# Kernel optimization log

Measured on AMD Instinct MI355X. Metric: run time of the kernel, lower is better.

The kernel has to match this reference:

```python
import jax, jax.numpy as jnp
import numpy as np

N = 50000
E = 800000
IN_DIM = 128
HEADS = 8
OUT_DIM = 32
NEG_SLOPE = 0.2


def setup_inputs() -> dict:
    key = jax.random.key(0)
    k1, k2, k3, k4, k5 = jax.random.split(key, 5)
    x = jax.random.normal(k1, (N, IN_DIM), dtype=jnp.float32)
    edge_index = jax.random.randint(k2, (2, E), 0, N, dtype=jnp.int64)
    batch = jnp.zeros((N,), dtype=jnp.int64)
    # GATConv params: glorot-style scale
    W = jax.random.normal(k3, (IN_DIM, HEADS * OUT_DIM), dtype=jnp.float32) * (1.0 / np.sqrt(IN_DIM))
    att_src = jax.random.normal(k4, (HEADS, OUT_DIM), dtype=jnp.float32) * (1.0 / np.sqrt(OUT_DIM))
    att_dst = jax.random.normal(k5, (HEADS, OUT_DIM), dtype=jnp.float32) * (1.0 / np.sqrt(OUT_DIM))
    bias = jnp.zeros((OUT_DIM,), dtype=jnp.float32)
    return {"x": x, "edge_index": edge_index, "batch": batch,
            "W": W, "att_src": att_src, "att_dst": att_dst, "bias": bias}


def reference(x, edge_index, batch, W, att_src, att_dst, bias):
    n = x.shape[0]
    h = (x @ W).reshape(n, HEADS, OUT_DIM)            # [N, H, C]
    a_src = jnp.einsum('nhc,hc->nh', h, att_src)       # [N, H]
    a_dst = jnp.einsum('nhc,hc->nh', h, att_dst)       # [N, H]
    # add self-loops (PyG default add_self_loops=True)
    loops = jnp.arange(n, dtype=edge_index.dtype)
    src = jnp.concatenate([edge_index[0], loops])
    dst = jnp.concatenate([edge_index[1], loops])
    e = jax.nn.leaky_relu(a_src[src] + a_dst[dst], NEG_SLOPE)  # [E+N, H]
    # scatter-softmax over incoming edges of each dst node
    m = jax.ops.segment_max(e, dst, num_segments=n)    # [N, H]
    m = jax.lax.stop_gradient(m)
    ex = jnp.exp(e - m[dst])
    denom = jax.ops.segment_sum(ex, dst, num_segments=n)
    alpha = ex / denom[dst]                            # [E+N, H]
    msg = h[src] * alpha[..., None]                    # [E+N, H, C]
    out = jax.ops.segment_sum(msg, dst, num_segments=n)  # [N, H, C]
    out = out.mean(axis=1) + bias                      # concat=False -> head mean
    return out
```

## Files before the change

### kernel.cpp

```cpp
#include <hip/hip_runtime.h>
#include <hip/hip_bf16.h>

#define IN_DIM 128
#define HC 256
#define HEADS 8
#define OUT_DIM 32
#define NEG_SLOPE 0.2f
#define ELL_CAP 64

typedef unsigned short ushort_t;
typedef unsigned int uint_t;
typedef __attribute__((ext_vector_type(8))) short bf16x8;
typedef __attribute__((ext_vector_type(8))) unsigned short ushort8_t;
typedef __attribute__((ext_vector_type(4))) float floatx4;

__device__ inline ushort_t f2bf(float f) {
    uint_t u = __float_as_uint(f);
    u = (u + 0x7FFF + ((u >> 16) & 1)) >> 16;
    return (ushort_t)u;
}
__device__ inline float bf2f(ushort_t u) {
    return __uint_as_float(((uint_t)u) << 16);
}
__device__ inline uint_t pkbf(float a, float b) {
    __hip_bfloat162 t = __float22bfloat162_rn(make_float2(a, b));
    union { __hip_bfloat162 h; uint_t u; } c;
    c.h = t;
    return c.u;
}

__global__ __launch_bounds__(256) void prep_w_zero(const float* __restrict__ W,
                                                   ushort_t* __restrict__ Wf,
                                                   int* __restrict__ deg, int N) {
    const int t = blockIdx.x * 256 + threadIdx.x;
    for (int i = t; i < N; i += 4096) deg[i] = 0;

    int lane = t & 63;
    int ks = (t >> 6) & 3;
    int nt = t >> 8;
    int n = nt * 16 + (lane & 15);
    int k0 = ks * 32 + (lane >> 4) * 8;
    float v[8];
#pragma unroll
    for (int j = 0; j < 8; j++) v[j] = W[(size_t)(k0 + j) * HC + n];
    uint4 pk;
    pk.x = pkbf(v[0], v[1]);
    pk.y = pkbf(v[2], v[3]);
    pk.z = pkbf(v[4], v[5]);
    pk.w = pkbf(v[6], v[7]);
    *(uint4*)&Wf[(size_t)t * 8] = pk;
}

__global__ __launch_bounds__(256) void build_gemm(const float* __restrict__ x,
                                                  const ushort_t* __restrict__ Wf,
                                                  const float* __restrict__ att_s,
                                                  const float* __restrict__ att_d,
                                                  ushort_t* __restrict__ h2,
                                                  float* __restrict__ a_src,
                                                  float* __restrict__ a_dst,
                                                  const int* __restrict__ esrc,
                                                  const int* __restrict__ edst,
                                                  int* __restrict__ deg,
                                                  ushort_t* __restrict__ ell,
                                                  int N, int E, int nbuild) {
    __shared__ ushort_t xs[128 * 136];
    const int tid = threadIdx.x;

    if ((int)blockIdx.x < nbuild) {
        int i = blockIdx.x * 256 + tid;
        int base = i * 4;
        if (base + 3 < E) {
            int4 d = *(const int4*)&edst[base];
            int4 s = *(const int4*)&esrc[base];
            int r0 = atomicAdd(&deg[d.x], 1);
            int r1 = atomicAdd(&deg[d.y], 1);
            int r2 = atomicAdd(&deg[d.z], 1);
            int r3 = atomicAdd(&deg[d.w], 1);
            if (r0 < ELL_CAP) ell[d.x * ELL_CAP + r0] = (ushort_t)s.x;
            if (r1 < ELL_CAP) ell[d.y * ELL_CAP + r1] = (ushort_t)s.y;
            if (r2 < ELL_CAP) ell[d.z * ELL_CAP + r2] = (ushort_t)s.z;
            if (r3 < ELL_CAP) ell[d.w * ELL_CAP + r3] = (ushort_t)s.w;
        } else if (base < E) {
            for (int j = base; j < E; j++) {
                int r = atomicAdd(&deg[edst[j]], 1);
                if (r < ELL_CAP) ell[edst[j] * ELL_CAP + r] = (ushort_t)esrc[j];
            }
        }
        return;
    }

    const int row0 = ((int)blockIdx.x - nbuild) * 128;
#pragma unroll
    for (int i = 0; i < 16; i++) {
        int slot = tid + i * 256;
        int r = slot >> 5, kq = slot & 31;
        int gr = row0 + r;
        float4 v = (gr < N) ? *(const float4*)&x[(size_t)gr * IN_DIM + kq * 4]
                            : make_float4(0.f, 0.f, 0.f, 0.f);
        uint2 pk;
        pk.x = pkbf(v.x, v.y);
        pk.y = pkbf(v.z, v.w);
        *(uint2*)&xs[r * 136 + kq * 4] = pk;
    }
    __syncthreads();

    const int lane = tid & 63;
    const int w = tid >> 6;
    const int wrow = (w & 1) * 64;
    const int wcol = (w >> 1) * 64;
    const int m15 = lane & 15, quad = lane >> 4;

#pragma unroll
    for (int ch = 0; ch < 2; ch++) {
        const int colblk = wcol + ch * 128;
        floatx4 acc[4][4] = {};
#pragma unroll
        for (int ks = 0; ks < 4; ks++) {
            bf16x8 xb[4], wa[4];
#pragma unroll
            for (int rt = 0; rt < 4; rt++)
                xb[rt] = *(const bf16x8*)&xs[(wrow + rt * 16 + m15) * 136 + ks * 32 + quad * 8];
#pragma unroll
            for (int ct = 0; ct < 4; ct++) {
                int mtg = (colblk >> 4) + ct;
                wa[ct] = *(const bf16x8*)&Wf[(size_t)(((mtg * 4 + ks) * 64) + lane) * 8];
            }
#pragma unroll
            for (int ct = 0; ct < 4; ct++)
#pragma unroll
                for (int rt = 0; rt < 4; rt++)
                    acc[ct][rt] = __builtin_amdgcn_mfma_f32_16x16x32_bf16(wa[ct], xb[rt], acc[ct][rt], 0, 0, 0);
        }

        const int hb = colblk >> 5;
        float asc[4][4], adc[4][4];
#pragma unroll
        for (int ct = 0; ct < 4; ct++)
#pragma unroll
            for (int reg = 0; reg < 4; reg++) {
                asc[ct][reg] = att_s[colblk + ct * 16 + quad * 4 + reg];
                adc[ct][reg] = att_d[colblk + ct * 16 + quad * 4 + reg];
            }
#pragma unroll
        for (int rt = 0; rt < 4; rt++) {
            int gr = row0 + wrow + rt * 16 + m15;
            bool ok = (gr < N);
            if (ok) {
#pragma unroll
                for (int ct = 0; ct < 4; ct++) {
                    uint2 pk;
                    pk.x = pkbf(acc[ct][rt][0], acc[ct][rt][1]);
                    pk.y = pkbf(acc[ct][rt][2], acc[ct][rt][3]);
                    *(uint2*)&h2[(size_t)gr * HC + colblk + ct * 16 + quad * 4] = pk;
                }
            }
            float sA = 0.f, sB = 0.f, dA = 0.f, dB = 0.f;
#pragma unroll
            for (int reg = 0; reg < 4; reg++) {
                sA += acc[0][rt][reg] * asc[0][reg] + acc[1][rt][reg] * asc[1][reg];
                sB += acc[2][rt][reg] * asc[2][reg] + acc[3][rt][reg] * asc[3][reg];
                dA += acc[0][rt][reg] * adc[0][reg] + acc[1][rt][reg] * adc[1][reg];
                dB += acc[2][rt][reg] * adc[2][reg] + acc[3][rt][reg] * adc[3][reg];
            }
            sA += __shfl_xor(sA, 16, 64); sA += __shfl_xor(sA, 32, 64);
            sB += __shfl_xor(sB, 16, 64); sB += __shfl_xor(sB, 32, 64);
            dA += __shfl_xor(dA, 16, 64); dA += __shfl_xor(dA, 32, 64);
            dB += __shfl_xor(dB, 16, 64); dB += __shfl_xor(dB, 32, 64);
            if (ok && quad == 0) {
                a_src[gr * HEADS + hb]     = sA;
                a_src[gr * HEADS + hb + 1] = sB;
                a_dst[gr * HEADS + hb]     = dA;
                a_dst[gr * HEADS + hb + 1] = dB;
            }
        }
    }
}

__global__ __launch_bounds__(256) void aggregate(const ushort_t* __restrict__ h2,
                                                 const float* __restrict__ a_src,
                                                 const float* __restrict__ a_dst,
                                                 const int* __restrict__ deg,
                                                 const ushort_t* __restrict__ ell,
                                                 const float* __restrict__ bias,
                                                 float* __restrict__ out, int N) {
    int wave = threadIdx.x >> 6;
    int lane = threadIdx.x & 63;
    int n = blockIdx.x * 4 + wave;
    if (n >= N) return;
    int half = lane >> 5;
    int sl = lane & 31;
    int head = sl >> 2;
    int rowoff = sl * 8;

    float adst = a_dst[n * HEADS + head];
    float e = a_src[n * HEADS + head] + adst;
    e = fmaxf(e, NEG_SLOPE * e);
    float p = (half == 0) ? __expf(e) : 0.f;
    ushort8_t hv = *(const ushort8_t*)&h2[(size_t)n * HC + rowoff];
    float acc[8];
#pragma unroll
    for (int j = 0; j < 8; j++) acc[j] = p * bf2f(hv[j]);
    float l = p;

    int dn = __builtin_amdgcn_readfirstlane(deg[n]);
    if (dn > ELL_CAP) dn = ELL_CAP;
    const ushort_t* row = &ell[(size_t)n * ELL_CAP];
    int k = 0;
    for (; k + 7 < dn; k += 8) {
        int sidx[4];
        float ev[4];
        ushort8_t g[4];
#pragma unroll
        for (int j = 0; j < 4; j++) sidx[j] = (int)row[k + 2 * j + half];
#pragma unroll
        for (int j = 0; j < 4; j++) {
            g[j] = *(const ushort8_t*)&h2[(size_t)sidx[j] * HC + rowoff];
            ev[j] = a_src[sidx[j] * HEADS + head];
        }
#pragma unroll
        for (int j = 0; j < 4; j++) {
            float ej = ev[j] + adst;
            ej = fmaxf(ej, NEG_SLOPE * ej);
            float pj = __expf(ej);
#pragma unroll
            for (int c = 0; c < 8; c++) acc[c] += pj * bf2f(g[j][c]);
            l += pj;
        }
    }
    for (; k + 1 < dn; k += 2) {
        int s0 = (int)row[k + half];
        float e0 = a_src[s0 * HEADS + head] + adst;
        ushort8_t g0 = *(const ushort8_t*)&h2[(size_t)s0 * HC + rowoff];
        e0 = fmaxf(e0, NEG_SLOPE * e0);
        float p0 = __expf(e0);
#pragma unroll
        for (int c = 0; c < 8; c++) acc[c] += p0 * bf2f(g0[c]);
        l += p0;
    }
    if (k < dn) {
        int s0 = (int)row[k];
        float e0 = a_src[s0 * HEADS + head] + adst;
        ushort8_t g0 = *(const ushort8_t*)&h2[(size_t)s0 * HC + rowoff];
        e0 = fmaxf(e0, NEG_SLOPE * e0);
        float p0 = (half == 0) ? __expf(e0) : 0.f;
#pragma unroll
        for (int c = 0; c < 8; c++) acc[c] += p0 * bf2f(g0[c]);
        l += p0;
    }

#pragma unroll
    for (int j = 0; j < 8; j++) acc[j] += __shfl_xor(acc[j], 32, 64);
    l += __shfl_xor(l, 32, 64);

    float inv = 0.125f / l;
#pragma unroll
    for (int j = 0; j < 8; j++) acc[j] *= inv;
#pragma unroll
    for (int off = 4; off < 32; off <<= 1)
#pragma unroll
        for (int j = 0; j < 8; j++) acc[j] += __shfl_xor(acc[j], off, 64);

    if (lane < 4) {
        int c8 = sl * 8;
        float4 b0 = *(const float4*)&bias[c8];
        float4 b1 = *(const float4*)&bias[c8 + 4];
        float4 o0 = make_float4(acc[0] + b0.x, acc[1] + b0.y, acc[2] + b0.z, acc[3] + b0.w);
        float4 o1 = make_float4(acc[4] + b1.x, acc[5] + b1.y, acc[6] + b1.z, acc[7] + b1.w);
        *(float4*)&out[(size_t)n * OUT_DIM + c8] = o0;
        *(float4*)&out[(size_t)n * OUT_DIM + c8 + 4] = o1;
    }
}

extern "C" void kernel_launch(void* const* d_in, const int* in_sizes, int n_in,
                              void* d_out, int out_size, void* d_ws, size_t ws_size,
                              hipStream_t stream) {
    const float* x       = (const float*)d_in[0];
    const int*   eidx    = (const int*)d_in[1];
    const float* W       = (const float*)d_in[3];
    const float* att_src = (const float*)d_in[4];
    const float* att_dst = (const float*)d_in[5];
    const float* bias    = (const float*)d_in[6];
    float* out = (float*)d_out;

    const int N = in_sizes[0] / IN_DIM;
    const int E = in_sizes[1] / 2;
    const int* esrc = eidx;
    const int* edst = eidx + E;

    char* wsb = (char*)d_ws;
    size_t off = 0;
    auto alloc = [&](size_t bytes) -> void* {
        void* p = wsb + off;
        off = (off + bytes + 255) & ~(size_t)255;
        return p;
    };
    ushort_t* h2   = (ushort_t*)alloc((size_t)N * HC * 2);
    ushort_t* Wf   = (ushort_t*)alloc((size_t)IN_DIM * HC * 2);
    float*    a_src= (float*)alloc((size_t)N * HEADS * 4);
    float*    a_dst= (float*)alloc((size_t)N * HEADS * 4);
    int*      deg  = (int*)alloc((size_t)N * 4);
    ushort_t* ell  = (ushort_t*)alloc((size_t)N * ELL_CAP * 2);

    const int nbuild = (E / 4 + 255) / 256;
    const int ngemm  = (N + 127) / 128;

    hipLaunchKernelGGL(prep_w_zero, dim3(16), dim3(256), 0, stream, W, Wf, deg, N);
    hipLaunchKernelGGL(build_gemm, dim3(nbuild + ngemm), dim3(256), 0, stream,
                       x, Wf, att_src, att_dst, h2, a_src, a_dst,
                       esrc, edst, deg, ell, N, E, nbuild);
    hipLaunchKernelGGL(aggregate, dim3((N + 3) / 4), dim3(256), 0, stream,
                       h2, a_src, a_dst, deg, ell, bias, out, N);
}
```

Baseline: 211.7 us.

## Interleave ELL build into GEMM blocks via atomic work-stealing and two nodes per wave

The GEMM now uses 64-row tiles, one wave per 64-column block. After finishing its tile, every block, plus 512 extra blocks, pulls batches of edges from a global atomic counter and builds the ELL adjacency, eight edges per lane. The aggregate kernel now gives each half-wave its own node, processes eight neighbours per iteration with masking, and drops the cross-half reduction. The aim is to overlap the atomic-heavy ELL build with GEMM work and to raise utilisation in aggregation. In exchange it adds counter contention and per-half-wave divergence when neighbouring nodes have different degrees.

After: 282.3 us. 33.4% more time.

```diff
diff --git a/kernel.cpp b/kernel.cpp
--- a/kernel.cpp
+++ b/kernel.cpp
@@ -14,11 +14,6 @@
 typedef __attribute__((ext_vector_type(8))) unsigned short ushort8_t;
 typedef __attribute__((ext_vector_type(4))) float floatx4;
 
-__device__ inline ushort_t f2bf(float f) {
-    uint_t u = __float_as_uint(f);
-    u = (u + 0x7FFF + ((u >> 16) & 1)) >> 16;
-    return (ushort_t)u;
-}
 __device__ inline float bf2f(ushort_t u) {
     return __uint_as_float(((uint_t)u) << 16);
 }
@@ -31,14 +26,16 @@
 
 __global__ __launch_bounds__(256) void prep_w_zero(const float* __restrict__ W,
                                                    ushort_t* __restrict__ Wf,
-                                                   int* __restrict__ deg, int N) {
+                                                   int* __restrict__ deg,
+                                                   int* __restrict__ ctr, int N) {
     const int t = blockIdx.x * 256 + threadIdx.x;
     for (int i = t; i < N; i += 4096) deg[i] = 0;
+    if (t == 0) *ctr = 0;
 
     int lane = t & 63;
     int ks = (t >> 6) & 3;
-    int nt = t >> 8;
-    int n = nt * 16 + (lane & 15);
+    int nt2 = t >> 8;
+    int n = nt2 * 16 + (lane & 15);
     int k0 = ks * 32 + (lane >> 4) * 8;
     float v[8];
 #pragma unroll
@@ -51,7 +48,7 @@
     *(uint4*)&Wf[(size_t)t * 8] = pk;
 }
 
-__global__ __launch_bounds__(256) void build_gemm(const float* __restrict__ x,
+__global__ __launch_bounds__(256) void gemm_build(const float* __restrict__ x,
                                                   const ushort_t* __restrict__ Wf,
                                                   const float* __restrict__ att_s,
                                                   const float* __restrict__ att_d,
@@ -62,64 +59,39 @@
                                                   const int* __restrict__ edst,
                                                   int* __restrict__ deg,
                                                   ushort_t* __restrict__ ell,
-                                                  int N, int E, int nbuild) {
-    __shared__ ushort_t xs[128 * 136];
+                                                  int* __restrict__ ctr,
+                                                  int N, int E, int ntiles) {
+    __shared__ ushort_t xs[64 * 136];
     const int tid = threadIdx.x;
-
-    if ((int)blockIdx.x < nbuild) {
-        int i = blockIdx.x * 256 + tid;
-        int base = i * 4;
-        if (base + 3 < E) {
-            int4 d = *(const int4*)&edst[base];
-            int4 s = *(const int4*)&esrc[base];
-            int r0 = atomicAdd(&deg[d.x], 1);
-            int r1 = atomicAdd(&deg[d.y], 1);
-            int r2 = atomicAdd(&deg[d.z], 1);
-            int r3 = atomicAdd(&deg[d.w], 1);
-            if (r0 < ELL_CAP) ell[d.x * ELL_CAP + r0] = (ushort_t)s.x;
-            if (r1 < ELL_CAP) ell[d.y * ELL_CAP + r1] = (ushort_t)s.y;
-            if (r2 < ELL_CAP) ell[d.z * ELL_CAP + r2] = (ushort_t)s.z;
-            if (r3 < ELL_CAP) ell[d.w * ELL_CAP + r3] = (ushort_t)s.w;
-        } else if (base < E) {
-            for (int j = base; j < E; j++) {
-                int r = atomicAdd(&deg[edst[j]], 1);
-                if (r < ELL_CAP) ell[edst[j] * ELL_CAP + r] = (ushort_t)esrc[j];
-            }
-        }
-        return;
-    }
-
-    const int row0 = ((int)blockIdx.x - nbuild) * 128;
-#pragma unroll
-    for (int i = 0; i < 16; i++) {
-        int slot = tid + i * 256;
-        int r = slot >> 5, kq = slot & 31;
-        int gr = row0 + r;
-        float4 v = (gr < N) ? *(const float4*)&x[(size_t)gr * IN_DIM + kq * 4]
-                            : make_float4(0.f, 0.f, 0.f, 0.f);
-        uint2 pk;
-        pk.x = pkbf(v.x, v.y);
-        pk.y = pkbf(v.z, v.w);
-        *(uint2*)&xs[r * 136 + kq * 4] = pk;
-    }
-    __syncthreads();
-
+    const int bid = blockIdx.x;
     const int lane = tid & 63;
     const int w = tid >> 6;
-    const int wrow = (w & 1) * 64;
-    const int wcol = (w >> 1) * 64;
-    const int m15 = lane & 15, quad = lane >> 4;
-
-#pragma unroll
-    for (int ch = 0; ch < 2; ch++) {
-        const int colblk = wcol + ch * 128;
+
+    if (bid < ntiles) {
+        const int row0 = bid * 64;
+        const int m15 = lane & 15, quad = lane >> 4;
+        const int colblk = w * 64;
+#pragma unroll
+        for (int i = 0; i < 8; i++) {
+            int slot = tid + i * 256;
+            int r = slot >> 5, kq = slot & 31;
+            int gr = row0 + r;
+            float4 v = (gr < N) ? *(const float4*)&x[(size_t)gr * IN_DIM + kq * 4]
+                                : make_float4(0.f, 0.f, 0.f, 0.f);
+            uint2 pk;
+            pk.x = pkbf(v.x, v.y);
+            pk.y = pkbf(v.z, v.w);
+            *(uint2*)&xs[r * 136 + kq * 4] = pk;
+        }
+        __syncthreads();
+
         floatx4 acc[4][4] = {};
 #pragma unroll
         for (int ks = 0; ks < 4; ks++) {
             bf16x8 xb[4], wa[4];
 #pragma unroll
             for (int rt = 0; rt < 4; rt++)
-                xb[rt] = *(const bf16x8*)&xs[(wrow + rt * 16 + m15) * 136 + ks * 32 + quad * 8];
+                xb[rt] = *(const bf16x8*)&xs[(rt * 16 + m15) * 136 + ks * 32 + quad * 8];
 #pragma unroll
             for (int ct = 0; ct < 4; ct++) {
                 int mtg = (colblk >> 4) + ct;
@@ -143,7 +115,7 @@
             }
 #pragma unroll
         for (int rt = 0; rt < 4; rt++) {
-            int gr = row0 + wrow + rt * 16 + m15;
+            int gr = row0 + rt * 16 + m15;
             bool ok = (gr < N);
             if (ok) {
 #pragma unroll
@@ -174,6 +146,46 @@
             }
         }
     }
+
+    const int nchunk = (E + 7) >> 3;
+    const int nbatch = (nchunk + 63) >> 6;
+    for (;;) {
+        int batch = 0;
+        if (lane == 0) batch = atomicAdd(ctr, 1);
+        batch = __shfl(batch, 0, 64);
+        if (batch >= nbatch) break;
+        int c = batch * 64 + lane;
+        if (c < nchunk) {
+            int base = c * 8;
+            if (base + 7 < E) {
+                int4 d0 = *(const int4*)&edst[base];
+                int4 d1 = *(const int4*)&edst[base + 4];
+                int4 s0 = *(const int4*)&esrc[base];
+                int4 s1 = *(const int4*)&esrc[base + 4];
+                int r0 = atomicAdd(&deg[d0.x], 1);
+                int r1 = atomicAdd(&deg[d0.y], 1);
+                int r2 = atomicAdd(&deg[d0.z], 1);
+                int r3 = atomicAdd(&deg[d0.w], 1);
+                int r4 = atomicAdd(&deg[d1.x], 1);
+                int r5 = atomicAdd(&deg[d1.y], 1);
+                int r6 = atomicAdd(&deg[d1.z], 1);
+                int r7 = atomicAdd(&deg[d1.w], 1);
+                if (r0 < ELL_CAP) ell[d0.x * ELL_CAP + r0] = (ushort_t)s0.x;
+                if (r1 < ELL_CAP) ell[d0.y * ELL_CAP + r1] = (ushort_t)s0.y;
+                if (r2 < ELL_CAP) ell[d0.z * ELL_CAP + r2] = (ushort_t)s0.z;
+                if (r3 < ELL_CAP) ell[d0.w * ELL_CAP + r3] = (ushort_t)s0.w;
+                if (r4 < ELL_CAP) ell[d1.x * ELL_CAP + r4] = (ushort_t)s1.x;
+                if (r5 < ELL_CAP) ell[d1.y * ELL_CAP + r5] = (ushort_t)s1.y;
+                if (r6 < ELL_CAP) ell[d1.z * ELL_CAP + r6] = (ushort_t)s1.z;
+                if (r7 < ELL_CAP) ell[d1.w * ELL_CAP + r7] = (ushort_t)s1.w;
+            } else {
+                for (int j = base; j < E; j++) {
+                    int r = atomicAdd(&deg[edst[j]], 1);
+                    if (r < ELL_CAP) ell[edst[j] * ELL_CAP + r] = (ushort_t)esrc[j];
+                }
+            }
+        }
+    }
 }
 
 __global__ __launch_bounds__(256) void aggregate(const ushort_t* __restrict__ h2,
@@ -183,74 +195,59 @@
                                                  const ushort_t* __restrict__ ell,
                                                  const float* __restrict__ bias,
                                                  float* __restrict__ out, int N) {
-    int wave = threadIdx.x >> 6;
-    int lane = threadIdx.x & 63;
-    int n = blockIdx.x * 4 + wave;
-    if (n >= N) return;
-    int half = lane >> 5;
-    int sl = lane & 31;
-    int head = sl >> 2;
-    int rowoff = sl * 8;
-
-    float adst = a_dst[n * HEADS + head];
-    float e = a_src[n * HEADS + head] + adst;
-    e = fmaxf(e, NEG_SLOPE * e);
-    float p = (half == 0) ? __expf(e) : 0.f;
-    ushort8_t hv = *(const ushort8_t*)&h2[(size_t)n * HC + rowoff];
+    const int wave = threadIdx.x >> 6;
+    const int lane = threadIdx.x & 63;
+    const int half = lane >> 5;
+    const int sl = lane & 31;
+    const int head = sl >> 2;
+    const int rowoff = sl * 8;
+
+    const int node = blockIdx.x * 8 + wave * 2 + half;
+    const bool nok = (node < N);
+    const int nd = nok ? node : 0;
+
+    float adst = a_dst[nd * HEADS + head];
+    float e0 = a_src[nd * HEADS + head] + adst;
+    e0 = fmaxf(e0, NEG_SLOPE * e0);
+    float p = __expf(e0);
+    ushort8_t hv = *(const ushort8_t*)&h2[(size_t)nd * HC + rowoff];
     float acc[8];
 #pragma unroll
     for (int j = 0; j < 8; j++) acc[j] = p * bf2f(hv[j]);
     float l = p;
 
-    int dn = __builtin_amdgcn_readfirstlane(deg[n]);
+    int dn = deg[nd];
     if (dn > ELL_CAP) dn = ELL_CAP;
-    const ushort_t* row = &ell[(size_t)n * ELL_CAP];
-    int k = 0;
-    for (; k + 7 < dn; k += 8) {
-        int sidx[4];
-        float ev[4];
-        ushort8_t g[4];
-#pragma unroll
-        for (int j = 0; j < 4; j++) sidx[j] = (int)row[k + 2 * j + half];
-#pragma unroll
-        for (int j = 0; j < 4; j++) {
+    const ushort_t* row = &ell[(size_t)nd * ELL_CAP];
+
+    for (int k = 0; k < dn; k += 8) {
+        int sidx[8];
+        float ev[8];
+        ushort8_t g[8];
+        bool vm[8];
+#pragma unroll
+        for (int j = 0; j < 8; j++) {
+            int kj = k + j;
+            vm[j] = (kj < dn);
+            int slot = (kj < ELL_CAP) ? kj : (ELL_CAP - 1);
+            int s = (int)row[slot];
+            sidx[j] = vm[j] ? s : 0;
+        }
+#pragma unroll
+        for (int j = 0; j < 8; j++) {
             g[j] = *(const ushort8_t*)&h2[(size_t)sidx[j] * HC + rowoff];
             ev[j] = a_src[sidx[j] * HEADS + head];
         }
 #pragma unroll
-        for (int j = 0; j < 4; j++) {
+        for (int j = 0; j < 8; j++) {
             float ej = ev[j] + adst;
             ej = fmaxf(ej, NEG_SLOPE * ej);
-            float pj = __expf(ej);
+            float pj = vm[j] ? __expf(ej) : 0.f;
 #pragma unroll
             for (int c = 0; c < 8; c++) acc[c] += pj * bf2f(g[j][c]);
             l += pj;
         }
     }
-    for (; k + 1 < dn; k += 2) {
-        int s0 = (int)row[k + half];
-        float e0 = a_src[s0 * HEADS + head] + adst;
-        ushort8_t g0 = *(const ushort8_t*)&h2[(size_t)s0 * HC + rowoff];
-        e0 = fmaxf(e0, NEG_SLOPE * e0);
-        float p0 = __expf(e0);
-#pragma unroll
-        for (int c = 0; c < 8; c++) acc[c] += p0 * bf2f(g0[c]);
-        l += p0;
-    }
-    if (k < dn) {
-        int s0 = (int)row[k];
-        float e0 = a_src[s0 * HEADS + head] + adst;
-        ushort8_t g0 = *(const ushort8_t*)&h2[(size_t)s0 * HC + rowoff];
-        e0 = fmaxf(e0, NEG_SLOPE * e0);
-        float p0 = (half == 0) ? __expf(e0) : 0.f;
-#pragma unroll
-        for (int c = 0; c < 8; c++) acc[c] += p0 * bf2f(g0[c]);
-        l += p0;
-    }
-
-#pragma unroll
-    for (int j = 0; j < 8; j++) acc[j] += __shfl_xor(acc[j], 32, 64);
-    l += __shfl_xor(l, 32, 64);
 
     float inv = 0.125f / l;
 #pragma unroll
@@ -260,14 +257,14 @@
 #pragma unroll
         for (int j = 0; j < 8; j++) acc[j] += __shfl_xor(acc[j], off, 64);
 
-    if (lane < 4) {
+    if (nok && sl < 4) {
         int c8 = sl * 8;
         float4 b0 = *(const float4*)&bias[c8];
         float4 b1 = *(const float4*)&bias[c8 + 4];
         float4 o0 = make_float4(acc[0] + b0.x, acc[1] + b0.y, acc[2] + b0.z, acc[3] + b0.w);
         float4 o1 = make_float4(acc[4] + b1.x, acc[5] + b1.y, acc[6] + b1.z, acc[7] + b1.w);
-        *(float4*)&out[(size_t)n * OUT_DIM + c8] = o0;
-        *(float4*)&out[(size_t)n * OUT_DIM + c8 + 4] = o1;
+        *(float4*)&out[(size_t)node * OUT_DIM + c8] = o0;
+        *(float4*)&out[(size_t)node * OUT_DIM + c8 + 4] = o1;
     }
 }
 
@@ -300,14 +297,15 @@
     float*    a_dst= (float*)alloc((size_t)N * HEADS * 4);
     int*      deg  = (int*)alloc((size_t)N * 4);
     ushort_t* ell  = (ushort_t*)alloc((size_t)N * ELL_CAP * 2);
-
-    const int nbuild = (E / 4 + 255) / 256;
-    const int ngemm  = (N + 127) / 128;
-
-    hipLaunchKernelGGL(prep_w_zero, dim3(16), dim3(256), 0, stream, W, Wf, deg, N);
-    hipLaunchKernelGGL(build_gemm, dim3(nbuild + ngemm), dim3(256), 0, stream,
+    int*      ctr  = (int*)alloc(256);
+
+    const int ntiles = (N + 63) / 64;
+    const int nblk2  = ntiles + 512;
+
+    hipLaunchKernelGGL(prep_w_zero, dim3(16), dim3(256), 0, stream, W, Wf, deg, ctr, N);
+    hipLaunchKernelGGL(gemm_build, dim3(nblk2), dim3(256), 0, stream,
                        x, Wf, att_src, att_dst, h2, a_src, a_dst,
-                       esrc, edst, deg, ell, N, E, nbuild);
-    hipLaunchKernelGGL(aggregate, dim3((N + 3) / 4), dim3(256), 0, stream,
+                       esrc, edst, deg, ell, ctr, N, E, ntiles);
+    hipLaunchKernelGGL(aggregate, dim3((N + 7) / 8), dim3(256), 0, stream,
                        h2, a_src, a_dst, deg, ell, bias, out, N);
 }
```
